# Optimization experiments

Measured on AMD Instinct MI355X. Metric: run time of the kernel, lower is better.

The kernel has to match this reference:

```python
import jax, jax.numpy as jnp
import numpy as np

B, S, D = 4, 2048, 1024

def setup_inputs() -> dict:
    key = jax.random.key(0)
    ks = jax.random.split(key, 7)
    scale = 1.0 / np.sqrt(D)
    return {
        "x": jax.random.normal(ks[0], (B, S, D), dtype=jnp.float32),
        "Wq": jax.random.uniform(ks[1], (D, D), jnp.float32, -scale, scale),
        "bq": jax.random.uniform(ks[2], (D,), jnp.float32, -scale, scale),
        "Wk": jax.random.uniform(ks[3], (D, D), jnp.float32, -scale, scale),
        "bk": jax.random.uniform(ks[4], (D,), jnp.float32, -scale, scale),
        "Wv": jax.random.uniform(ks[5], (D, D), jnp.float32, -scale, scale),
        "bv": jax.random.uniform(ks[6], (D,), jnp.float32, -scale, scale),
    }

def reference(x, Wq, bq, Wk, bk, Wv, bv):
    # Linear layers: x @ W^T + b (torch nn.Linear convention)
    q = jnp.einsum('bsd,ed->bse', x, Wq) + bq  # [B,S,D]
    k = jnp.einsum('bsd,ed->bse', x, Wk) + bk
    v = jnp.einsum('bsd,ed->bse', x, Wv) + bv
    inv_sqrt_d = 1.0 / jnp.sqrt(jnp.asarray(k.shape[-1], k.dtype))
    scores = jnp.einsum('bqd,bkd->bqk', q, k) * inv_sqrt_d  # [B,S,S]
    attn = jax.nn.softmax(scores, axis=-1)
    return jnp.einsum('bqk,bkd->bqd', attn, v)
```

## Files before the change

### kernel.cpp

```cpp
#include <hip/hip_runtime.h>
#include <cstdint>


typedef __bf16 bf16x8_t __attribute__((ext_vector_type(8)));
typedef float  f32x4_t  __attribute__((ext_vector_type(4)));

__device__ __forceinline__ uint16_t f2bf(float f) {
    union { float f; uint32_t u; } v; v.f = f;
    return (uint16_t)((v.u + 0x7fffu + ((v.u >> 16) & 1u)) >> 16);
}

__device__ __forceinline__ void gload_lds16(const uint16_t* g, uint16_t* lds) {
    __builtin_amdgcn_global_load_lds(
        (const __attribute__((address_space(1))) void*)g,
        (__attribute__((address_space(3))) void*)lds, 16, 0, 0);
}

template <int EPI, typename OutT>
__global__ __launch_bounds__(256, 4) void gemm_bt(
    const uint16_t* __restrict__ A, int lda, long long sAz,
    const uint16_t* __restrict__ B, int ldb, long long sBz,
    OutT* __restrict__ C, int ldc, long long sCz,
    const float* __restrict__ bias0, const float* __restrict__ bias1,
    float* __restrict__ gsum, int K, float alpha)
{
    __shared__ uint16_t ldsA[128 * 64];
    __shared__ uint16_t ldsB[128 * 64];
    __shared__ float inv_denom[128];

    const int tid  = threadIdx.x;
    const int wave = tid >> 6;
    const int lane = tid & 63;
    const int quad = lane >> 4;
    const int l15  = lane & 15;
    const int z    = blockIdx.z;

    A += (long long)z * sAz;
    B += (long long)z * sBz;
    C += (long long)z * sCz;

    const int m0 = blockIdx.x * 128;
    const int n0 = blockIdx.y * 128;

    if (EPI == 4) {
        if (tid < 128) {
            const float* gp = gsum + (long long)z * 32768 + (m0 + tid) * 16;
            float s = 0.f;
#pragma unroll
            for (int t = 0; t < 16; ++t) s += gp[t];
            inv_denom[tid] = 1.f / s;
        }
    }

    const uint16_t* gA[4];
    const uint16_t* gB[4];
    uint16_t* lA[4];
    uint16_t* lB[4];
#pragma unroll
    for (int c = 0; c < 4; ++c) {
        const int s   = (c * 4 + wave) * 64 + lane;
        const int r   = s >> 3;
        const int col = ((s & 7) ^ (r & 7)) * 8;
        gA[c] = A + (long long)(m0 + r) * lda + col;
        gB[c] = B + (long long)(n0 + r) * ldb + col;
        lA[c] = ldsA + (c * 4 + wave) * 512;
        lB[c] = ldsB + (c * 4 + wave) * 512;
    }

    const int m_off = (wave & 1) * 64;
    const int n_off = (wave >> 1) * 64;

    f32x4_t acc[4][4];
#pragma unroll
    for (int i = 0; i < 4; ++i)
#pragma unroll
        for (int j = 0; j < 4; ++j)
            acc[i][j] = f32x4_t{0.f, 0.f, 0.f, 0.f};

    for (int k0 = 0; k0 < K; k0 += 64) {
#pragma unroll
        for (int c = 0; c < 4; ++c) gload_lds16(gA[c], lA[c]);
#pragma unroll
        for (int c = 0; c < 4; ++c) gload_lds16(gB[c], lB[c]);
#pragma unroll
        for (int c = 0; c < 4; ++c) { gA[c] += 64; gB[c] += 64; }
        __syncthreads();

#pragma unroll
        for (int t = 0; t < 2; ++t) {
            const int csw = ((t * 4 + quad) ^ (l15 & 7)) * 8;
            bf16x8_t af[4], bfr[4];
#pragma unroll
            for (int i = 0; i < 4; ++i)
                af[i] = *(const bf16x8_t*)(ldsA + (m_off + i * 16 + l15) * 64 + csw);
#pragma unroll
            for (int j = 0; j < 4; ++j)
                bfr[j] = *(const bf16x8_t*)(ldsB + (n_off + j * 16 + l15) * 64 + csw);
#pragma unroll
            for (int i = 0; i < 4; ++i)
#pragma unroll
                for (int j = 0; j < 4; ++j)
                    acc[i][j] = __builtin_amdgcn_mfma_f32_16x16x32_bf16(af[i], bfr[j], acc[i][j], 0, 0, 0);
        }
        __syncthreads();
    }

    if (EPI == 1 || EPI == 2) {
        const float* bias = (z == 0) ? bias0 : bias1;
#pragma unroll
        for (int i = 0; i < 4; ++i) {
            const int mb = m0 + m_off + i * 16 + quad * 4;
            float rb[4];
            if (EPI == 2) {
#pragma unroll
                for (int r = 0; r < 4; ++r) rb[r] = bias[mb + r];
            }
#pragma unroll
            for (int j = 0; j < 4; ++j) {
                const int n = n0 + n_off + j * 16 + l15;
                const float cb = (EPI == 1) ? bias[n] : 0.f;
#pragma unroll
                for (int r = 0; r < 4; ++r) {
                    float v = acc[i][j][r] + ((EPI == 1) ? cb : rb[r]);
                    ((uint16_t*)C)[(long long)(mb + r) * ldc + n] = f2bf(v);
                }
            }
        }
    } else if (EPI == 3) {
        float rs[4][4];
#pragma unroll
        for (int i = 0; i < 4; ++i)
#pragma unroll
            for (int r = 0; r < 4; ++r) rs[i][r] = 0.f;
#pragma unroll
        for (int i = 0; i < 4; ++i) {
            const int mb = m0 + m_off + i * 16 + quad * 4;
#pragma unroll
            for (int j = 0; j < 4; ++j) {
                const int n = n0 + n_off + j * 16 + l15;
#pragma unroll
                for (int r = 0; r < 4; ++r) {
                    const float e = exp2f(acc[i][j][r] * alpha);
                    rs[i][r] += e;
                    ((uint16_t*)C)[(long long)(mb + r) * ldc + n] = f2bf(e);
                }
            }
        }
#pragma unroll
        for (int m = 1; m < 16; m <<= 1)
#pragma unroll
            for (int i = 0; i < 4; ++i)
#pragma unroll
                for (int r = 0; r < 4; ++r)
                    rs[i][r] += __shfl_xor(rs[i][r], m);
        float* lp = (float*)ldsA;
        if (l15 == 0) {
#pragma unroll
            for (int i = 0; i < 4; ++i)
#pragma unroll
                for (int r = 0; r < 4; ++r)
                    lp[wave * 64 + i * 16 + quad * 4 + r] = rs[i][r];
        }
        __syncthreads();
        if (tid < 128) {
            const float s = lp[(tid >> 6) * 64 + (tid & 63)] +
                            lp[((tid >> 6) + 2) * 64 + (tid & 63)];
            gsum[(long long)z * 32768 + (m0 + tid) * 16 + blockIdx.y] = s;
        }
    } else {
#pragma unroll
        for (int i = 0; i < 4; ++i) {
            const int rl = m_off + i * 16 + quad * 4;
            const int mb = m0 + rl;
#pragma unroll
            for (int j = 0; j < 4; ++j) {
                const int n = n0 + n_off + j * 16 + l15;
#pragma unroll
                for (int r = 0; r < 4; ++r)
                    ((float*)C)[(long long)(mb + r) * ldc + n] =
                        acc[i][j][r] * inv_denom[rl + r];
            }
        }
    }
}

__global__ void cvt_all(const float* __restrict__ x,
                        const float* __restrict__ Wq, const float* __restrict__ Wk,
                        const float* __restrict__ Wv,
                        uint16_t* __restrict__ x_bf, uint16_t* __restrict__ w_bf) {
    const int b = blockIdx.x;
    const float* src;
    uint16_t* dst;
    int i;
    if (b < 8192) {
        src = x; dst = x_bf; i = b * 256 + threadIdx.x;
    } else {
        const int wz = (b - 8192) >> 10;
        const int rb = (b - 8192) & 1023;
        src = (wz == 0) ? Wq : (wz == 1) ? Wk : Wv;
        dst = w_bf + (long long)wz * 1048576;
        i = rb * 256 + threadIdx.x;
    }
    const float4 f = ((const float4*)src)[i];
    ushort4 o;
    o.x = f2bf(f.x); o.y = f2bf(f.y); o.z = f2bf(f.z); o.w = f2bf(f.w);
    ((ushort4*)dst)[i] = o;
}

extern "C" void kernel_launch(void* const* d_in, const int* in_sizes, int n_in,
                              void* d_out, int out_size, void* d_ws, size_t ws_size,
                              hipStream_t stream) {
    const float* x  = (const float*)d_in[0];
    const float* Wq = (const float*)d_in[1];
    const float* bq = (const float*)d_in[2];
    const float* Wk = (const float*)d_in[3];
    const float* bk = (const float*)d_in[4];
    const float* Wv = (const float*)d_in[5];
    const float* bv = (const float*)d_in[6];
    float* out = (float*)d_out;

    char* w = (char*)d_ws;
    uint16_t* x_bf = (uint16_t*)(w);
    float*    gsum = (float*)(w);
    uint16_t* w_bf = (uint16_t*)(w + 16777216);
    uint16_t* Qb   = (uint16_t*)(w + 23068672);
    uint16_t* Kb   = (uint16_t*)(w + 39845888);
    uint16_t* Vt   = (uint16_t*)(w + 56623104);
    uint16_t* Pb   = (uint16_t*)(w + 73400320);

    cvt_all<<<11264, 256, 0, stream>>>(x, Wq, Wk, Wv, x_bf, w_bf);

    gemm_bt<1, uint16_t><<<dim3(64, 8, 2), 256, 0, stream>>>(
        x_bf, 1024, 0LL,
        w_bf, 1024, 1048576LL,
        Qb, 1024, 8388608LL,
        bq, bk, nullptr, 1024, 1.0f);

    gemm_bt<2, uint16_t><<<dim3(8, 64, 1), 256, 0, stream>>>(
        w_bf + 2097152, 1024, 0LL,
        x_bf, 1024, 0LL,
        Vt, 8192, 0LL,
        bv, bv, nullptr, 1024, 1.0f);

    gemm_bt<3, uint16_t><<<dim3(16, 16, 4), 256, 0, stream>>>(
        Qb, 1024, 2097152LL,
        Kb, 1024, 2097152LL,
        Pb, 2048, 4194304LL,
        nullptr, nullptr, gsum, 1024, 0.045084222f);

    gemm_bt<4, float><<<dim3(16, 8, 4), 256, 0, stream>>>(
        Pb, 2048, 4194304LL,
        Vt, 8192, 2048LL,
        out, 1024, 2097152LL,
        nullptr, nullptr, gsum, 2048, 1.0f);
}
```

Measured before the change: 244.1 us.

## Store Q and K as FP8 and compute attention scores with FP8 scaled MFMA

The Q/K projection epilogue now writes FP8 (e4m3) instead of bf16, and a new score kernel computes QK^T with the 16x16x128 f8f6f4 scaled MFMA over 128-wide K tiles, keeping the exp and row-sum epilogue. This halves Q/K memory traffic and doubles MFMA throughput for the score GEMM. The cost is lower precision in the attention scores, which may push error past tolerance.

New measurement: 234.3 us. 1.04x faster.

```diff
diff --git a/kernel.cpp b/kernel.cpp
--- a/kernel.cpp
+++ b/kernel.cpp
@@ -4,13 +4,30 @@
 
 typedef __bf16 bf16x8_t __attribute__((ext_vector_type(8)));
 typedef float  f32x4_t  __attribute__((ext_vector_type(4)));
+typedef int    i32x8_t  __attribute__((ext_vector_type(8)));
+typedef int    i32x4_t  __attribute__((ext_vector_type(4)));
 
 __device__ __forceinline__ uint16_t f2bf(float f) {
     union { float f; uint32_t u; } v; v.f = f;
     return (uint16_t)((v.u + 0x7fffu + ((v.u >> 16) & 1u)) >> 16);
 }
 
-__device__ __forceinline__ void gload_lds16(const uint16_t* g, uint16_t* lds) {
+__device__ __forceinline__ uint8_t f2fp8(float f) {
+    union { float f; uint32_t u; } v; v.f = f;
+    const uint32_t sgn = (v.u >> 31) << 7;
+    const uint32_t mag = v.u & 0x7fffffffu;
+    uint32_t out;
+    if (mag < 0x3c800000u) {
+        out = (uint32_t)__builtin_rintf(__builtin_fabsf(f) * 512.0f);
+    } else {
+        uint32_t t = mag + 0x7ffffu + ((mag >> 20) & 1u);
+        out = (t >> 20) - 960u;
+        if (out > 0x7eu) out = 0x7eu;
+    }
+    return (uint8_t)(sgn | out);
+}
+
+__device__ __forceinline__ void gload_lds16(const void* g, void* lds) {
     __builtin_amdgcn_global_load_lds(
         (const __attribute__((address_space(1))) void*)g,
         (__attribute__((address_space(3))) void*)lds, 16, 0, 0);
@@ -121,51 +138,13 @@
                 const float cb = (EPI == 1) ? bias[n] : 0.f;
 #pragma unroll
                 for (int r = 0; r < 4; ++r) {
-                    float v = acc[i][j][r] + ((EPI == 1) ? cb : rb[r]);
-                    ((uint16_t*)C)[(long long)(mb + r) * ldc + n] = f2bf(v);
+                    const float v = acc[i][j][r] + ((EPI == 1) ? cb : rb[r]);
+                    if (sizeof(OutT) == 1)
+                        ((uint8_t*)C)[(long long)(mb + r) * ldc + n] = f2fp8(v);
+                    else
+                        ((uint16_t*)C)[(long long)(mb + r) * ldc + n] = f2bf(v);
                 }
             }
-        }
-    } else if (EPI == 3) {
-        float rs[4][4];
-#pragma unroll
-        for (int i = 0; i < 4; ++i)
-#pragma unroll
-            for (int r = 0; r < 4; ++r) rs[i][r] = 0.f;
-#pragma unroll
-        for (int i = 0; i < 4; ++i) {
-            const int mb = m0 + m_off + i * 16 + quad * 4;
-#pragma unroll
-            for (int j = 0; j < 4; ++j) {
-                const int n = n0 + n_off + j * 16 + l15;
-#pragma unroll
-                for (int r = 0; r < 4; ++r) {
-                    const float e = exp2f(acc[i][j][r] * alpha);
-                    rs[i][r] += e;
-                    ((uint16_t*)C)[(long long)(mb + r) * ldc + n] = f2bf(e);
-                }
-            }
-        }
-#pragma unroll
-        for (int m = 1; m < 16; m <<= 1)
-#pragma unroll
-            for (int i = 0; i < 4; ++i)
-#pragma unroll
-                for (int r = 0; r < 4; ++r)
-                    rs[i][r] += __shfl_xor(rs[i][r], m);
-        float* lp = (float*)ldsA;
-        if (l15 == 0) {
-#pragma unroll
-            for (int i = 0; i < 4; ++i)
-#pragma unroll
-                for (int r = 0; r < 4; ++r)
-                    lp[wave * 64 + i * 16 + quad * 4 + r] = rs[i][r];
-        }
-        __syncthreads();
-        if (tid < 128) {
-            const float s = lp[(tid >> 6) * 64 + (tid & 63)] +
-                            lp[((tid >> 6) + 2) * 64 + (tid & 63)];
-            gsum[(long long)z * 32768 + (m0 + tid) * 16 + blockIdx.y] = s;
         }
     } else {
 #pragma unroll
@@ -181,6 +160,135 @@
                         acc[i][j][r] * inv_denom[rl + r];
             }
         }
+    }
+}
+
+__global__ __launch_bounds__(256, 3) void score_f8(
+    const uint8_t* __restrict__ Qf8, const uint8_t* __restrict__ Kf8,
+    uint16_t* __restrict__ P, float* __restrict__ gsum, float alpha)
+{
+    __shared__ uint8_t ldsA[128 * 128];
+    __shared__ uint8_t ldsB[128 * 128];
+
+    const int tid  = threadIdx.x;
+    const int wave = tid >> 6;
+    const int lane = tid & 63;
+    const int quad = lane >> 4;
+    const int l15  = lane & 15;
+    const int z    = blockIdx.z;
+
+    const uint8_t* A = Qf8 + (long long)z * 2097152;
+    const uint8_t* B = Kf8 + (long long)z * 2097152;
+    uint16_t* C = P + (long long)z * 4194304;
+
+    const int m0 = blockIdx.x * 128;
+    const int n0 = blockIdx.y * 128;
+
+    const uint8_t* gA[4];
+    const uint8_t* gB[4];
+    uint8_t* lA[4];
+    uint8_t* lB[4];
+#pragma unroll
+    for (int c = 0; c < 4; ++c) {
+        const int s   = (c * 4 + wave) * 64 + lane;
+        const int r   = s >> 3;
+        const int col = ((s & 7) ^ (r & 7)) * 16;
+        gA[c] = A + (long long)(m0 + r) * 1024 + col;
+        gB[c] = B + (long long)(n0 + r) * 1024 + col;
+        lA[c] = ldsA + (c * 4 + wave) * 1024;
+        lB[c] = ldsB + (c * 4 + wave) * 1024;
+    }
+
+    const int m_off = (wave & 1) * 64;
+    const int n_off = (wave >> 1) * 64;
+
+    f32x4_t acc[4][4];
+#pragma unroll
+    for (int i = 0; i < 4; ++i)
+#pragma unroll
+        for (int j = 0; j < 4; ++j)
+            acc[i][j] = f32x4_t{0.f, 0.f, 0.f, 0.f};
+
+    const int h0 = quad * 2;
+    const int h1 = quad * 2 + 1;
+
+    for (int k0 = 0; k0 < 1024; k0 += 128) {
+#pragma unroll
+        for (int c = 0; c < 4; ++c) gload_lds16(gA[c], lA[c]);
+#pragma unroll
+        for (int c = 0; c < 4; ++c) gload_lds16(gB[c], lB[c]);
+#pragma unroll
+        for (int c = 0; c < 4; ++c) { gA[c] += 128; gB[c] += 128; }
+        __syncthreads();
+
+        i32x8_t af[4], bfr[4];
+#pragma unroll
+        for (int i = 0; i < 4; ++i) {
+            const int m = m_off + i * 16 + l15;
+            const int sw = m & 7;
+            const i32x4_t lo = *(const i32x4_t*)(ldsA + m * 128 + (h0 ^ sw) * 16);
+            const i32x4_t hi = *(const i32x4_t*)(ldsA + m * 128 + (h1 ^ sw) * 16);
+            af[i] = i32x8_t{lo[0], lo[1], lo[2], lo[3], hi[0], hi[1], hi[2], hi[3]};
+        }
+#pragma unroll
+        for (int j = 0; j < 4; ++j) {
+            const int n = n_off + j * 16 + l15;
+            const int sw = n & 7;
+            const i32x4_t lo = *(const i32x4_t*)(ldsB + n * 128 + (h0 ^ sw) * 16);
+            const i32x4_t hi = *(const i32x4_t*)(ldsB + n * 128 + (h1 ^ sw) * 16);
+            bfr[j] = i32x8_t{lo[0], lo[1], lo[2], lo[3], hi[0], hi[1], hi[2], hi[3]};
+        }
+#pragma unroll
+        for (int i = 0; i < 4; ++i)
+#pragma unroll
+            for (int j = 0; j < 4; ++j)
+                acc[i][j] = __builtin_amdgcn_mfma_scale_f32_16x16x128_f8f6f4(
+                    af[i], bfr[j], acc[i][j],
+                    0, 0,
+                    0, 0x7f7f7f7f,
+                    0, 0x7f7f7f7f);
+        __syncthreads();
+    }
+
+    float rs[4][4];
+#pragma unroll
+    for (int i = 0; i < 4; ++i)
+#pragma unroll
+        for (int r = 0; r < 4; ++r) rs[i][r] = 0.f;
+#pragma unroll
+    for (int i = 0; i < 4; ++i) {
+        const int mb = m0 + m_off + i * 16 + quad * 4;
+#pragma unroll
+        for (int j = 0; j < 4; ++j) {
+            const int n = n0 + n_off + j * 16 + l15;
+#pragma unroll
+            for (int r = 0; r < 4; ++r) {
+                const float e = exp2f(acc[i][j][r] * alpha);
+                rs[i][r] += e;
+                C[(long long)(mb + r) * 2048 + n] = f2bf(e);
+            }
+        }
+    }
+#pragma unroll
+    for (int m = 1; m < 16; m <<= 1)
+#pragma unroll
+        for (int i = 0; i < 4; ++i)
+#pragma unroll
+            for (int r = 0; r < 4; ++r)
+                rs[i][r] += __shfl_xor(rs[i][r], m);
+    float* lp = (float*)ldsA;
+    if (l15 == 0) {
+#pragma unroll
+        for (int i = 0; i < 4; ++i)
+#pragma unroll
+            for (int r = 0; r < 4; ++r)
+                lp[wave * 64 + i * 16 + quad * 4 + r] = rs[i][r];
+    }
+    __syncthreads();
+    if (tid < 128) {
+        const float s = lp[(tid >> 6) * 64 + (tid & 63)] +
+                        lp[((tid >> 6) + 2) * 64 + (tid & 63)];
+        gsum[(long long)z * 32768 + (m0 + tid) * 16 + blockIdx.y] = s;
     }
 }
 
@@ -223,17 +331,17 @@
     uint16_t* x_bf = (uint16_t*)(w);
     float*    gsum = (float*)(w);
     uint16_t* w_bf = (uint16_t*)(w + 16777216);
-    uint16_t* Qb   = (uint16_t*)(w + 23068672);
-    uint16_t* Kb   = (uint16_t*)(w + 39845888);
-    uint16_t* Vt   = (uint16_t*)(w + 56623104);
-    uint16_t* Pb   = (uint16_t*)(w + 73400320);
+    uint8_t*  Qf8  = (uint8_t*)(w + 23068672);
+    uint8_t*  Kf8  = (uint8_t*)(w + 31457280);
+    uint16_t* Vt   = (uint16_t*)(w + 39845888);
+    uint16_t* Pb   = (uint16_t*)(w + 56623104);
 
     cvt_all<<<11264, 256, 0, stream>>>(x, Wq, Wk, Wv, x_bf, w_bf);
 
-    gemm_bt<1, uint16_t><<<dim3(64, 8, 2), 256, 0, stream>>>(
+    gemm_bt<1, uint8_t><<<dim3(64, 8, 2), 256, 0, stream>>>(
         x_bf, 1024, 0LL,
         w_bf, 1024, 1048576LL,
-        Qb, 1024, 8388608LL,
+        Qf8, 1024, 8388608LL,
         bq, bk, nullptr, 1024, 1.0f);
 
     gemm_bt<2, uint16_t><<<dim3(8, 64, 1), 256, 0, stream>>>(
@@ -242,11 +350,8 @@
         Vt, 8192, 0LL,
         bv, bv, nullptr, 1024, 1.0f);
 
-    gemm_bt<3, uint16_t><<<dim3(16, 16, 4), 256, 0, stream>>>(
-        Qb, 1024, 2097152LL,
-        Kb, 1024, 2097152LL,
-        Pb, 2048, 4194304LL,
-        nullptr, nullptr, gsum, 1024, 0.045084222f);
+    score_f8<<<dim3(16, 16, 4), 256, 0, stream>>>(
+        Qf8, Kf8, Pb, gsum, 0.045084222f);
 
     gemm_bt<4, float><<<dim3(16, 8, 4), 256, 0, stream>>>(
         Pb, 2048, 4194304LL,
```
